# Kernel optimization log

Hardware: AMD Instinct MI355X
Metric: run time of the kernel (lower is better)

## Reference

```python
import jax, jax.numpy as jnp
import numpy as np

R = 2          # upscale factor (init kwarg r)
CHANNELS = 64  # output channels (init kwarg channels); input C = CHANNELS * R * R


def setup_inputs() -> dict:
    key = jax.random.key(0)
    x = jax.random.normal(key, (8, 256, 256, CHANNELS * R * R), dtype=jnp.float32)
    return {"x": x}


def reference(x) -> jnp.ndarray:
    # Faithful to SubPixelUpscaling.PS / _phase_shift (TF backend, NHWC):
    # out[n, h*r + r1, w*r + r2, c] = x[n, h, w, c*r*r + r1*r + r2]
    B, H, W, C = x.shape
    r = R
    ch = C // (r * r)
    # (B,H,W,ch,r,r) -> (B,H,r1,W,r2,ch) -> (B,H*r,W*r,ch)
    y = x.reshape(B, H, W, ch, r, r)
    y = y.transpose(0, 1, 4, 2, 5, 3)
    return y.reshape(B, H * r, W * r, ch)
```

## Files before the change

### kernel.cpp

```cpp
#include <hip/hip_runtime.h>


typedef float f32x4 __attribute__((ext_vector_type(4)));

__global__ __launch_bounds__(256) void SubPixelUpscaling_kernel(
    const float* __restrict__ in, float* __restrict__ out, int npairs) {
    __shared__ __align__(16) float lds[4][2][256];

    const int lane = threadIdx.x & 63;
    const int wid  = threadIdx.x >> 6;
    const int gw   = blockIdx.x * 4 + wid;
    const int nw   = gridDim.x * 4;

    float* const row0 = &lds[wid][0][0];
    float* const row1 = &lds[wid][1][0];
    const int l4 = lane << 2;

    for (int pair = gw; pair < npairs; pair += nw) {
        const int p = pair << 1;
        const int w = p & 255;
        const int h = (p >> 8) & 255;
        const int n = p >> 16;

        const f32x4 vA = *reinterpret_cast<const f32x4*>(in + (p << 8) + l4);
        const f32x4 vB = *reinterpret_cast<const f32x4*>(in + ((p + 1) << 8) + l4);

        row0[lane]       = vA.x;
        row0[64 + lane]  = vA.y;
        row0[128 + lane] = vB.x;
        row0[192 + lane] = vB.y;
        row1[lane]       = vA.z;
        row1[64 + lane]  = vA.w;
        row1[128 + lane] = vB.z;
        row1[192 + lane] = vB.w;

        asm volatile("s_waitcnt lgkmcnt(0)" ::: "memory");

        const f32x4 r0 = *reinterpret_cast<const f32x4*>(row0 + l4);
        const f32x4 r1 = *reinterpret_cast<const f32x4*>(row1 + l4);

        const int ob = ((((n << 9) + (h << 1)) << 9) + (w << 1)) << 6;
        *reinterpret_cast<f32x4*>(out + ob + l4)         = r0;
        *reinterpret_cast<f32x4*>(out + ob + 32768 + l4) = r1;
    }
}

extern "C" void kernel_launch(void* const* d_in, const int* in_sizes, int n_in,
                              void* d_out, int out_size, void* d_ws, size_t ws_size,
                              hipStream_t stream) {
    const float* in = (const float*)d_in[0];
    float* out = (float*)d_out;

    const int npairs = (out_size / 4) / 128;
    const int block = 256;
    const int grid  = 2048;

    SubPixelUpscaling_kernel<<<grid, block, 0, stream>>>(in, out, npairs);
}
```

Before: 219.8 us.

## Process four pixels per iteration with register prefetch and nontemporal memory ops

Each wave now handles four input pixels per loop iteration instead of two, doubling LDS staging. The next iteration's loads are issued into registers before the current iteration's shuffle and stores, overlapping load latency with work. Loads and stores use nontemporal hints to avoid cache pollution on this streaming copy. This raises register and LDS use per wave, and the kernel is already near memory bandwidth.

Measured after the change: 184.1 us. 1.19x faster.

```diff
diff --git a/kernel.cpp b/kernel.cpp
--- a/kernel.cpp
+++ b/kernel.cpp
@@ -4,8 +4,8 @@
 typedef float f32x4 __attribute__((ext_vector_type(4)));
 
 __global__ __launch_bounds__(256) void SubPixelUpscaling_kernel(
-    const float* __restrict__ in, float* __restrict__ out, int npairs) {
-    __shared__ __align__(16) float lds[4][2][256];
+    const float* __restrict__ in, float* __restrict__ out, int nquads) {
+    __shared__ __align__(16) float lds[4][2][512];
 
     const int lane = threadIdx.x & 63;
     const int wid  = threadIdx.x >> 6;
@@ -15,33 +15,57 @@
     float* const row0 = &lds[wid][0][0];
     float* const row1 = &lds[wid][1][0];
     const int l4 = lane << 2;
+    const float* const inl = in + l4;
 
-    for (int pair = gw; pair < npairs; pair += nw) {
-        const int p = pair << 1;
+    int q = gw;
+    if (q >= nquads) return;
+
+    f32x4 a0 = __builtin_nontemporal_load(reinterpret_cast<const f32x4*>(inl + ((q << 2) << 8)));
+    f32x4 a1 = __builtin_nontemporal_load(reinterpret_cast<const f32x4*>(inl + (((q << 2) + 1) << 8)));
+    f32x4 a2 = __builtin_nontemporal_load(reinterpret_cast<const f32x4*>(inl + (((q << 2) + 2) << 8)));
+    f32x4 a3 = __builtin_nontemporal_load(reinterpret_cast<const f32x4*>(inl + (((q << 2) + 3) << 8)));
+
+    while (true) {
+        const int next = q + nw;
+        f32x4 b0, b1, b2, b3;
+        const bool have_next = next < nquads;
+        if (have_next) {
+            b0 = __builtin_nontemporal_load(reinterpret_cast<const f32x4*>(inl + ((next << 2) << 8)));
+            b1 = __builtin_nontemporal_load(reinterpret_cast<const f32x4*>(inl + (((next << 2) + 1) << 8)));
+            b2 = __builtin_nontemporal_load(reinterpret_cast<const f32x4*>(inl + (((next << 2) + 2) << 8)));
+            b3 = __builtin_nontemporal_load(reinterpret_cast<const f32x4*>(inl + (((next << 2) + 3) << 8)));
+        }
+
+        const int p = q << 2;
         const int w = p & 255;
         const int h = (p >> 8) & 255;
         const int n = p >> 16;
 
-        const f32x4 vA = *reinterpret_cast<const f32x4*>(in + (p << 8) + l4);
-        const f32x4 vB = *reinterpret_cast<const f32x4*>(in + ((p + 1) << 8) + l4);
-
-        row0[lane]       = vA.x;
-        row0[64 + lane]  = vA.y;
-        row0[128 + lane] = vB.x;
-        row0[192 + lane] = vB.y;
-        row1[lane]       = vA.z;
-        row1[64 + lane]  = vA.w;
-        row1[128 + lane] = vB.z;
-        row1[192 + lane] = vB.w;
+        row0[lane]       = a0.x;  row0[64  + lane] = a0.y;
+        row0[128 + lane] = a1.x;  row0[192 + lane] = a1.y;
+        row0[256 + lane] = a2.x;  row0[320 + lane] = a2.y;
+        row0[384 + lane] = a3.x;  row0[448 + lane] = a3.y;
+        row1[lane]       = a0.z;  row1[64  + lane] = a0.w;
+        row1[128 + lane] = a1.z;  row1[192 + lane] = a1.w;
+        row1[256 + lane] = a2.z;  row1[320 + lane] = a2.w;
+        row1[384 + lane] = a3.z;  row1[448 + lane] = a3.w;
 
         asm volatile("s_waitcnt lgkmcnt(0)" ::: "memory");
 
-        const f32x4 r0 = *reinterpret_cast<const f32x4*>(row0 + l4);
-        const f32x4 r1 = *reinterpret_cast<const f32x4*>(row1 + l4);
+        const f32x4 r0a = *reinterpret_cast<const f32x4*>(row0 + l4);
+        const f32x4 r0b = *reinterpret_cast<const f32x4*>(row0 + 256 + l4);
+        const f32x4 r1a = *reinterpret_cast<const f32x4*>(row1 + l4);
+        const f32x4 r1b = *reinterpret_cast<const f32x4*>(row1 + 256 + l4);
 
         const int ob = ((((n << 9) + (h << 1)) << 9) + (w << 1)) << 6;
-        *reinterpret_cast<f32x4*>(out + ob + l4)         = r0;
-        *reinterpret_cast<f32x4*>(out + ob + 32768 + l4) = r1;
+        __builtin_nontemporal_store(r0a, reinterpret_cast<f32x4*>(out + ob + l4));
+        __builtin_nontemporal_store(r0b, reinterpret_cast<f32x4*>(out + ob + 256 + l4));
+        __builtin_nontemporal_store(r1a, reinterpret_cast<f32x4*>(out + ob + 32768 + l4));
+        __builtin_nontemporal_store(r1b, reinterpret_cast<f32x4*>(out + ob + 32768 + 256 + l4));
+
+        if (!have_next) break;
+        a0 = b0; a1 = b1; a2 = b2; a3 = b3;
+        q = next;
     }
 }
 
@@ -51,9 +75,9 @@
     const float* in = (const float*)d_in[0];
     float* out = (float*)d_out;
 
-    const int npairs = (out_size / 4) / 128;
+    const int nquads = (out_size / 4) / 256;
     const int block = 256;
     const int grid  = 2048;
 
-    SubPixelUpscaling_kernel<<<grid, block, 0, stream>>>(in, out, npairs);
+    SubPixelUpscaling_kernel<<<grid, block, 0, stream>>>(in, out, nquads);
 }
```
